# Performance work log

Measured on AMD Instinct MI355X. Metric: run time of the kernel, lower is better.

The kernel has to match this reference:

```python
import jax, jax.numpy as jnp
import numpy as np

ETA = 0.15
LAM = 0.05
K = 6


def setup_inputs() -> dict:
    key = jax.random.key(0)
    ks = jax.random.split(key, 9)
    Bsz, L, d, hidden = 32, 8192, 64, 256
    scale = lambda fan_in: 1.0 / np.sqrt(fan_in)
    return {
        "A": jax.random.normal(ks[0], (Bsz, L, d), jnp.float32),
        "B": jax.random.normal(ks[1], (Bsz, L, d), jnp.float32),
        "q": jax.random.normal(ks[2], (Bsz, L, d), jnp.float32),
        "W1": jax.random.normal(ks[3], (2 * d, hidden), jnp.float32) * scale(2 * d),
        "b1": jax.random.normal(ks[4], (hidden,), jnp.float32) * 0.01,
        "W2": jax.random.normal(ks[5], (hidden, d), jnp.float32) * scale(hidden),
        "b2": jax.random.normal(ks[6], (d,), jnp.float32) * 0.01,
        "Wq": jax.random.normal(ks[7], (d, d), jnp.float32) * scale(d),
        "bq": jax.random.normal(ks[8], (d,), jnp.float32) * 0.01,
    }


def _smooth1d(x):
    return x - LAM * (2.0 * x - jnp.roll(x, 1, axis=1) - jnp.roll(x, -1, axis=1))


def reference(A, B, q, W1, b1, W2, b2, Wq, bq):
    # mu_net: Linear -> ReLU -> Linear -> Softplus on concat([A,B])
    h = jnp.concatenate([A, B], axis=-1)  # [B, L, 2d]
    mu = jax.nn.softplus(jax.nn.relu(h @ W1 + b1) @ W2 + b2)  # [B, L, d]
    gate = jnp.tanh(q @ Wq + bq)
    mu = mu * (1.0 + 0.5 * gate)

    hA, hB = A, B
    for _ in range(K):
        step = ETA * (mu * (hA - hB))
        hA = _smooth1d(hA - step)
        hB = _smooth1d(hB + step)

    energy = 0.5 * jnp.sum(mu * jnp.square(hA - hB), axis=(1, 2))  # [B]
    return hA, hB, energy
```

## Files before the change

kernel.cpp:

```cpp
#include <hip/hip_runtime.h>
#include <hip/hip_bf16.h>
#include <hip/hip_fp16.h>

#define ETA 0.15f
#define LAM 0.05f

typedef unsigned int uint32;
typedef __attribute__((ext_vector_type(8))) short short8;
typedef __attribute__((ext_vector_type(4))) float floatx4;
typedef __attribute__((ext_vector_type(2))) uint32 uint32x2;
typedef __attribute__((ext_vector_type(4))) _Float16 half4;

static const int BSZ = 32, LL = 8192, DD = 64;
static const int RTOT = BSZ * LL;

static const size_t MU_BYTES = (size_t)RTOT * DD * 2;
static const size_t W1T_OFF  = MU_BYTES;
static const size_t W2T_OFF  = W1T_OFF + 256 * 128 * 2;
static const size_t WQT_OFF  = W2T_OFF + 64 * 256 * 2;

__device__ __forceinline__ unsigned short f2bf(float f) {
    uint32 u = __builtin_bit_cast(uint32, f);
    uint32 r = (u + 0x7FFFu + ((u >> 16) & 1u)) >> 16;
    return (unsigned short)r;
}
__device__ __forceinline__ uint32 cvtpk(float lo, float hi) {
    uint32 r;
    asm("v_cvt_pk_bf16_f32 %0, %1, %2" : "=v"(r) : "v"(lo), "v"(hi));
    return r;
}
__device__ __forceinline__ float fast_softplus(float x) {
    return fmaxf(x, 0.f) + __logf(1.f + __expf(-fabsf(x)));
}
__device__ __forceinline__ float fast_tanh(float x) {
    float t = __expf(-2.f * fabsf(x));
    float r = (1.f - t) / (1.f + t);
    return copysignf(r, x);
}

__global__ void prep_kernel(const float* __restrict__ W1, const float* __restrict__ W2,
                            const float* __restrict__ Wq,
                            unsigned short* __restrict__ w1t, unsigned short* __restrict__ w2t,
                            unsigned short* __restrict__ wqt, float* __restrict__ energy) {
    int tid = blockIdx.x * blockDim.x + threadIdx.x;
    int nth = gridDim.x * blockDim.x;
    for (int i = tid; i < 256 * 128; i += nth) { int n = i >> 7, k = i & 127; w1t[i] = f2bf(W1[k * 256 + n]); }
    for (int i = tid; i < 64 * 256; i += nth) { int n = i >> 8, k = i & 255; w2t[i] = f2bf(W2[k * 64 + n]); }
    for (int i = tid; i < 64 * 64;  i += nth) { int n = i >> 6, k = i & 63;  wqt[i] = f2bf(Wq[k * 64 + n]); }
    if (tid < 32) energy[tid] = 0.f;
}

__global__ __launch_bounds__(256) void mlp_kernel(
    const float* __restrict__ A, const float* __restrict__ B, const float* __restrict__ Q,
    const float* __restrict__ b1, const float* __restrict__ b2, const float* __restrict__ bq,
    const unsigned short* __restrict__ w1t, const unsigned short* __restrict__ w2t,
    const unsigned short* __restrict__ wqt, _Float16* __restrict__ mu_out) {
    __shared__ char lds[32768];
    unsigned short* Xs = (unsigned short*)(lds);
    unsigned short* Qs = (unsigned short*)(lds + 17408);
    unsigned short* Zs = (unsigned short*)(lds);

    const int tid = threadIdx.x;
    const int lane = tid & 63;
    const int w = tid >> 6;
    const int q4 = lane >> 4;
    const int l16 = lane & 15;
    const int rowbase = blockIdx.x * 64;

    short8 wqf[2];
#pragma unroll
    for (int kt = 0; kt < 2; kt++)
        wqf[kt] = *(const short8*)&wqt[(w * 16 + l16) * 64 + kt * 32 + q4 * 8];
    float b1v4[4];
#pragma unroll
    for (int nt = 0; nt < 4; nt++) b1v4[nt] = b1[(w * 4 + nt) * 16 + l16];
    const int ocol = w * 16 + l16;
    const float b2v = b2[ocol], bqv = bq[ocol];

    uint32* Xu = (uint32*)Xs;
    for (int i = tid; i < 64 * 32; i += 256) {
        int r = i >> 5, c = i & 31;
        const float* src = (c < 16) ? (A + (size_t)(rowbase + r) * 64 + c * 4)
                                    : (B + (size_t)(rowbase + r) * 64 + (c - 16) * 4);
        floatx4 v = *(const floatx4*)src;
        uint32x2 u; u.x = cvtpk(v.x, v.y); u.y = cvtpk(v.z, v.w);
        *(uint32x2*)&Xu[r * 68 + c * 2] = u;
    }
    uint32* Qu = (uint32*)Qs;
    for (int i = tid; i < 64 * 16; i += 256) {
        int r = i >> 4, c = i & 15;
        floatx4 v = *(const floatx4*)(Q + (size_t)(rowbase + r) * 64 + c * 4);
        uint32x2 u; u.x = cvtpk(v.x, v.y); u.y = cvtpk(v.z, v.w);
        *(uint32x2*)&Qu[r * 36 + c * 2] = u;
    }
    __syncthreads();

    floatx4 acc3[4];
#pragma unroll
    for (int m = 0; m < 4; m++) acc3[m] = (floatx4){0.f, 0.f, 0.f, 0.f};
    __builtin_amdgcn_s_setprio(1);
#pragma unroll
    for (int m = 0; m < 4; m++)
#pragma unroll
        for (int kt = 0; kt < 2; kt++) {
            short8 aq = *(const short8*)&Qs[(m * 16 + l16) * 72 + kt * 32 + q4 * 8];
            acc3[m] = __builtin_amdgcn_mfma_f32_16x16x32_bf16(aq, wqf[kt], acc3[m], 0, 0, 0);
        }
    __builtin_amdgcn_s_setprio(0);
    short8 ax[4][4];
#pragma unroll
    for (int m = 0; m < 4; m++)
#pragma unroll
        for (int kt = 0; kt < 4; kt++)
            ax[m][kt] = *(const short8*)&Xs[(m * 16 + l16) * 136 + kt * 32 + q4 * 8];
    __syncthreads();

#pragma unroll
    for (int nt = 0; nt < 4; nt++) {
        const int ng = w * 4 + nt;
        short8 wf[4];
#pragma unroll
        for (int kt = 0; kt < 4; kt++)
            wf[kt] = *(const short8*)&w1t[(ng * 16 + l16) * 128 + kt * 32 + q4 * 8];
        floatx4 acc[4];
#pragma unroll
        for (int m = 0; m < 4; m++) acc[m] = (floatx4){0.f, 0.f, 0.f, 0.f};
        __builtin_amdgcn_s_setprio(1);
#pragma unroll
        for (int kt = 0; kt < 4; kt++)
#pragma unroll
            for (int m = 0; m < 4; m++)
                acc[m] = __builtin_amdgcn_mfma_f32_16x16x32_bf16(ax[m][kt], wf[kt], acc[m], 0, 0, 0);
        __builtin_amdgcn_s_setprio(0);
        const int col = ng * 16 + l16;
        const int c8 = col >> 3, c7 = col & 7;
        const float b1v = b1v4[nt];
#pragma unroll
        for (int m = 0; m < 4; m++) {
            float z0 = fmaxf(acc[m][0] + b1v, 0.f);
            float z1 = fmaxf(acc[m][1] + b1v, 0.f);
            float z2 = fmaxf(acc[m][2] + b1v, 0.f);
            float z3 = fmaxf(acc[m][3] + b1v, 0.f);
            uint32 u01 = cvtpk(z0, z1), u23 = cvtpk(z2, z3);
            const int row0 = m * 16 + q4 * 4;
            const int a0 = row0 * 256 + ((c8 ^ (q4 * 2)) << 3) + c7;
            const int a2 = (row0 + 2) * 256 + ((c8 ^ (q4 * 2 + 1)) << 3) + c7;
            Zs[a0]       = (unsigned short)u01;
            Zs[a0 + 256] = (unsigned short)(u01 >> 16);
            Zs[a2]       = (unsigned short)u23;
            Zs[a2 + 256] = (unsigned short)(u23 >> 16);
        }
    }
    short8 w2f[8];
#pragma unroll
    for (int kt = 0; kt < 8; kt++)
        w2f[kt] = *(const short8*)&w2t[(w * 16 + l16) * 256 + kt * 32 + q4 * 8];
    __syncthreads();

    floatx4 acc2[4];
#pragma unroll
    for (int m = 0; m < 4; m++) acc2[m] = (floatx4){0.f, 0.f, 0.f, 0.f};
    const int sxr = (l16 >> 1) & 7;
    __builtin_amdgcn_s_setprio(1);
#pragma unroll
    for (int m = 0; m < 4; m++)
#pragma unroll
        for (int kt = 0; kt < 8; kt++) {
            short8 az = *(const short8*)&Zs[(m * 16 + l16) * 256 + (((kt * 4 + q4) ^ sxr) << 3)];
            acc2[m] = __builtin_amdgcn_mfma_f32_16x16x32_bf16(az, w2f[kt], acc2[m], 0, 0, 0);
        }
    __builtin_amdgcn_s_setprio(0);
#pragma unroll
    for (int m = 0; m < 4; m++)
#pragma unroll
        for (int r = 0; r < 4; r++) {
            int row = m * 16 + q4 * 4 + r;
            float sp = fast_softplus(acc2[m][r] + b2v);
            float g = fast_tanh(acc3[m][r] + bqv);
            float mu = sp * (1.f + 0.5f * g);
            mu_out[(size_t)(rowbase + row) * 64 + ocol] = (_Float16)mu;
        }
}

__global__ __launch_bounds__(256) void iter_kernel(
    const float* __restrict__ A, const float* __restrict__ B, const _Float16* __restrict__ mu_ws,
    float* __restrict__ outA, float* __restrict__ outB, float* __restrict__ energy) {
    __shared__ float ex[2][4][16][64];
    __shared__ float esm[4];
    const int tid = threadIdx.x;
    const int c4 = tid & 15;
    const int g = tid >> 4;
    const int b = blockIdx.y;
    const int s0 = blockIdx.x * 64;
    const size_t bbase = (size_t)b * 8192;
    const int r0 = g * 5;

    floatx4 sv[5], dv[5], fv[5];
#pragma unroll
    for (int i = 0; i < 5; i++) {
        int gl = (s0 + r0 + i + 8192 - 8) & 8191;
        size_t base = (bbase + gl) * 64 + c4 * 4;
        floatx4 av = *(const floatx4*)(A + base);
        floatx4 bv = *(const floatx4*)(B + base);
        half4 m4 = *(const half4*)(mu_ws + base);
        floatx4 mu = __builtin_convertvector(m4, floatx4);
        sv[i] = av + bv;
        dv[i] = av - bv;
        fv[i] = 1.f - (2.f * ETA) * mu;
    }
    for (int it = 0; it < 6; it++) {
#pragma unroll
        for (int i = 0; i < 5; i++) dv[i] *= fv[i];
        const int p = it & 1;
        *(floatx4*)&ex[p][0][g][c4 * 4] = sv[0];
        *(floatx4*)&ex[p][1][g][c4 * 4] = sv[4];
        *(floatx4*)&ex[p][2][g][c4 * 4] = dv[0];
        *(floatx4*)&ex[p][3][g][c4 * 4] = dv[4];
        __syncthreads();
        floatx4 sUp = (g > 0)  ? *(const floatx4*)&ex[p][1][g - 1][c4 * 4] : sv[0];
        floatx4 sDn = (g < 15) ? *(const floatx4*)&ex[p][0][g + 1][c4 * 4] : sv[4];
        floatx4 dUp = (g > 0)  ? *(const floatx4*)&ex[p][3][g - 1][c4 * 4] : dv[0];
        floatx4 dDn = (g < 15) ? *(const floatx4*)&ex[p][2][g + 1][c4 * 4] : dv[4];
        floatx4 prev = sUp, cur = sv[0];
#pragma unroll
        for (int i = 0; i < 5; i++) {
            floatx4 nxt = (i < 4) ? sv[i + 1] : sDn;
            sv[i] = cur - LAM * (2.f * cur - prev - nxt);
            prev = cur; cur = nxt;
        }
        prev = dUp; cur = dv[0];
#pragma unroll
        for (int i = 0; i < 5; i++) {
            floatx4 nxt = (i < 4) ? dv[i + 1] : dDn;
            dv[i] = cur - LAM * (2.f * cur - prev - nxt);
            prev = cur; cur = nxt;
        }
    }
    float e = 0.f;
#pragma unroll
    for (int i = 0; i < 5; i++) {
        int wr = r0 + i;
        if (wr >= 8 && wr < 72) {
            floatx4 d = dv[i];
            floatx4 q = (1.f - fv[i]) * d * d;
            e += q.x + q.y + q.z + q.w;
            size_t gidx = (bbase + s0 + (wr - 8)) * 64 + c4 * 4;
            *(floatx4*)(outA + gidx) = (sv[i] + d) * 0.5f;
            *(floatx4*)(outB + gidx) = (sv[i] - d) * 0.5f;
        }
    }
    e *= 0.25f / ETA;
#pragma unroll
    for (int off = 32; off > 0; off >>= 1) e += __shfl_down(e, off, 64);
    if ((tid & 63) == 0) esm[tid >> 6] = e;
    __syncthreads();
    if (tid == 0) atomicAdd(energy + b, esm[0] + esm[1] + esm[2] + esm[3]);
}

extern "C" void kernel_launch(void* const* d_in, const int* in_sizes, int n_in,
                              void* d_out, int out_size, void* d_ws, size_t ws_size,
                              hipStream_t stream) {
    const float* A  = (const float*)d_in[0];
    const float* B  = (const float*)d_in[1];
    const float* Q  = (const float*)d_in[2];
    const float* W1 = (const float*)d_in[3];
    const float* b1 = (const float*)d_in[4];
    const float* W2 = (const float*)d_in[5];
    const float* b2 = (const float*)d_in[6];
    const float* Wq = (const float*)d_in[7];
    const float* bq = (const float*)d_in[8];

    float* outA = (float*)d_out;
    float* outB = outA + (size_t)RTOT * 64;
    float* energy = outB + (size_t)RTOT * 64;

    char* ws = (char*)d_ws;
    _Float16* mu_ws = (_Float16*)ws;
    unsigned short* w1t = (unsigned short*)(ws + W1T_OFF);
    unsigned short* w2t = (unsigned short*)(ws + W2T_OFF);
    unsigned short* wqt = (unsigned short*)(ws + WQT_OFF);

    hipLaunchKernelGGL(prep_kernel, dim3(64), dim3(256), 0, stream,
                       W1, W2, Wq, w1t, w2t, wqt, energy);
    hipLaunchKernelGGL(mlp_kernel, dim3(RTOT / 64), dim3(256), 0, stream,
                       A, B, Q, b1, b2, bq, w1t, w2t, wqt, mu_ws);
    hipLaunchKernelGGL(iter_kernel, dim3(LL / 64, BSZ), dim3(256), 0, stream,
                       A, B, mu_ws, outA, outB, energy);
}
```

Before: 396.1 us.

## Fuse MLP mu computation into stencil iteration kernel, keeping mu in LDS

Merges the MLP kernel and the iteration kernel into one. Each block computes mu for its 80-row haloed tile, with operands swapped so the MFMA output is transposed, and stores it as fp16 in LDS instead of a global workspace. This removes the fp16 mu write and read-back plus the second read of A and B. In exchange it recomputes the MLP on 16 halo rows per 64-row tile (about 25% extra matmul work), and the larger LDS footprint of about 64 KB limits occupancy to two blocks per CU.

```diff
diff --git a/kernel.cpp b/kernel.cpp
--- a/kernel.cpp
+++ b/kernel.cpp
@@ -1,5 +1,4 @@
 #include <hip/hip_runtime.h>
-#include <hip/hip_bf16.h>
 #include <hip/hip_fp16.h>
 
 #define ETA 0.15f
@@ -14,10 +13,9 @@
 static const int BSZ = 32, LL = 8192, DD = 64;
 static const int RTOT = BSZ * LL;
 
-static const size_t MU_BYTES = (size_t)RTOT * DD * 2;
-static const size_t W1T_OFF  = MU_BYTES;
-static const size_t W2T_OFF  = W1T_OFF + 256 * 128 * 2;
-static const size_t WQT_OFF  = W2T_OFF + 64 * 256 * 2;
+static const size_t W1T_OFF = 0;
+static const size_t W2T_OFF = W1T_OFF + 256 * 128 * 2;
+static const size_t WQT_OFF = W2T_OFF + 64 * 256 * 2;
 
 __device__ __forceinline__ unsigned short f2bf(float f) {
     uint32 u = __builtin_bit_cast(uint32, f);
@@ -50,105 +48,105 @@
     if (tid < 32) energy[tid] = 0.f;
 }
 
-__global__ __launch_bounds__(256) void mlp_kernel(
+__global__ __launch_bounds__(256, 2) void fused_kernel(
     const float* __restrict__ A, const float* __restrict__ B, const float* __restrict__ Q,
     const float* __restrict__ b1, const float* __restrict__ b2, const float* __restrict__ bq,
     const unsigned short* __restrict__ w1t, const unsigned short* __restrict__ w2t,
-    const unsigned short* __restrict__ wqt, _Float16* __restrict__ mu_out) {
-    __shared__ char lds[32768];
+    const unsigned short* __restrict__ wqt,
+    float* __restrict__ outA, float* __restrict__ outB, float* __restrict__ energy) {
+    __shared__ char lds[64048];
     unsigned short* Xs = (unsigned short*)(lds);
-    unsigned short* Qs = (unsigned short*)(lds + 17408);
-    unsigned short* Zs = (unsigned short*)(lds);
+    unsigned short* Qs = (unsigned short*)(lds + 21760);
+    unsigned short* Zs = (unsigned short*)(lds + 21760);
+    _Float16* muS = (_Float16*)(lds);
+    float* exb = (float*)(lds + 11264);
+    float* esm = (float*)(lds + 44032);
 
     const int tid = threadIdx.x;
     const int lane = tid & 63;
     const int w = tid >> 6;
     const int q4 = lane >> 4;
     const int l16 = lane & 15;
-    const int rowbase = blockIdx.x * 64;
+    const int g = tid >> 4;
+    const int c4 = tid & 15;
+    const int bb = blockIdx.y;
+    const int s0 = blockIdx.x * 64;
+    const size_t bbase = (size_t)bb * LL;
 
     short8 wqf[2];
 #pragma unroll
     for (int kt = 0; kt < 2; kt++)
         wqf[kt] = *(const short8*)&wqt[(w * 16 + l16) * 64 + kt * 32 + q4 * 8];
-    float b1v4[4];
-#pragma unroll
-    for (int nt = 0; nt < 4; nt++) b1v4[nt] = b1[(w * 4 + nt) * 16 + l16];
-    const int ocol = w * 16 + l16;
-    const float b2v = b2[ocol], bqv = bq[ocol];
-
+    floatx4 b1q[4];
+#pragma unroll
+    for (int ht = 0; ht < 4; ht++) b1q[ht] = *(const floatx4*)&b1[w * 64 + ht * 16 + q4 * 4];
+    const floatx4 b2q = *(const floatx4*)&b2[w * 16 + q4 * 4];
+    const floatx4 bqq = *(const floatx4*)&bq[w * 16 + q4 * 4];
+
+    floatx4 av[5], bv[5];
     uint32* Xu = (uint32*)Xs;
-    for (int i = tid; i < 64 * 32; i += 256) {
-        int r = i >> 5, c = i & 31;
-        const float* src = (c < 16) ? (A + (size_t)(rowbase + r) * 64 + c * 4)
-                                    : (B + (size_t)(rowbase + r) * 64 + (c - 16) * 4);
-        floatx4 v = *(const floatx4*)src;
-        uint32x2 u; u.x = cvtpk(v.x, v.y); u.y = cvtpk(v.z, v.w);
-        *(uint32x2*)&Xu[r * 68 + c * 2] = u;
-    }
     uint32* Qu = (uint32*)Qs;
-    for (int i = tid; i < 64 * 16; i += 256) {
-        int r = i >> 4, c = i & 15;
-        floatx4 v = *(const floatx4*)(Q + (size_t)(rowbase + r) * 64 + c * 4);
-        uint32x2 u; u.x = cvtpk(v.x, v.y); u.y = cvtpk(v.z, v.w);
-        *(uint32x2*)&Qu[r * 36 + c * 2] = u;
-    }
-    __syncthreads();
-
-    floatx4 acc3[4];
-#pragma unroll
-    for (int m = 0; m < 4; m++) acc3[m] = (floatx4){0.f, 0.f, 0.f, 0.f};
+#pragma unroll
+    for (int i = 0; i < 5; i++) {
+        int wr = g * 5 + i;
+        int gl = (s0 + wr + LL - 8) & (LL - 1);
+        size_t base = (bbase + gl) * 64 + c4 * 4;
+        av[i] = *(const floatx4*)(A + base);
+        bv[i] = *(const floatx4*)(B + base);
+        floatx4 qv = *(const floatx4*)(Q + base);
+        uint32x2 ua; ua.x = cvtpk(av[i].x, av[i].y); ua.y = cvtpk(av[i].z, av[i].w);
+        uint32x2 ub; ub.x = cvtpk(bv[i].x, bv[i].y); ub.y = cvtpk(bv[i].z, bv[i].w);
+        uint32x2 uq; uq.x = cvtpk(qv.x, qv.y);       uq.y = cvtpk(qv.z, qv.w);
+        *(uint32x2*)&Xu[wr * 68 + c4 * 2] = ua;
+        *(uint32x2*)&Xu[wr * 68 + 32 + c4 * 2] = ub;
+        *(uint32x2*)&Qu[wr * 36 + c4 * 2] = uq;
+    }
+    __syncthreads();
+
+    floatx4 acc3[5];
+#pragma unroll
+    for (int nt = 0; nt < 5; nt++) acc3[nt] = (floatx4){0.f, 0.f, 0.f, 0.f};
     __builtin_amdgcn_s_setprio(1);
 #pragma unroll
-    for (int m = 0; m < 4; m++)
+    for (int nt = 0; nt < 5; nt++)
 #pragma unroll
         for (int kt = 0; kt < 2; kt++) {
-            short8 aq = *(const short8*)&Qs[(m * 16 + l16) * 72 + kt * 32 + q4 * 8];
-            acc3[m] = __builtin_amdgcn_mfma_f32_16x16x32_bf16(aq, wqf[kt], acc3[m], 0, 0, 0);
+            short8 aq = *(const short8*)&Qs[(nt * 16 + l16) * 72 + kt * 32 + q4 * 8];
+            acc3[nt] = __builtin_amdgcn_mfma_f32_16x16x32_bf16(wqf[kt], aq, acc3[nt], 0, 0, 0);
         }
     __builtin_amdgcn_s_setprio(0);
-    short8 ax[4][4];
-#pragma unroll
-    for (int m = 0; m < 4; m++)
+    short8 ax[5][4];
+#pragma unroll
+    for (int nt = 0; nt < 5; nt++)
 #pragma unroll
         for (int kt = 0; kt < 4; kt++)
-            ax[m][kt] = *(const short8*)&Xs[(m * 16 + l16) * 136 + kt * 32 + q4 * 8];
-    __syncthreads();
-
-#pragma unroll
-    for (int nt = 0; nt < 4; nt++) {
-        const int ng = w * 4 + nt;
+            ax[nt][kt] = *(const short8*)&Xs[(nt * 16 + l16) * 136 + kt * 32 + q4 * 8];
+    __syncthreads();
+
+#pragma unroll
+    for (int ht = 0; ht < 4; ht++) {
         short8 wf[4];
 #pragma unroll
         for (int kt = 0; kt < 4; kt++)
-            wf[kt] = *(const short8*)&w1t[(ng * 16 + l16) * 128 + kt * 32 + q4 * 8];
-        floatx4 acc[4];
-#pragma unroll
-        for (int m = 0; m < 4; m++) acc[m] = (floatx4){0.f, 0.f, 0.f, 0.f};
+            wf[kt] = *(const short8*)&w1t[(w * 64 + ht * 16 + l16) * 128 + kt * 32 + q4 * 8];
+        floatx4 acc[5];
+#pragma unroll
+        for (int nt = 0; nt < 5; nt++) acc[nt] = (floatx4){0.f, 0.f, 0.f, 0.f};
         __builtin_amdgcn_s_setprio(1);
 #pragma unroll
         for (int kt = 0; kt < 4; kt++)
 #pragma unroll
-            for (int m = 0; m < 4; m++)
-                acc[m] = __builtin_amdgcn_mfma_f32_16x16x32_bf16(ax[m][kt], wf[kt], acc[m], 0, 0, 0);
+            for (int nt = 0; nt < 5; nt++)
+                acc[nt] = __builtin_amdgcn_mfma_f32_16x16x32_bf16(wf[kt], ax[nt][kt], acc[nt], 0, 0, 0);
         __builtin_amdgcn_s_setprio(0);
-        const int col = ng * 16 + l16;
-        const int c8 = col >> 3, c7 = col & 7;
-        const float b1v = b1v4[nt];
-#pragma unroll
-        for (int m = 0; m < 4; m++) {
-            float z0 = fmaxf(acc[m][0] + b1v, 0.f);
-            float z1 = fmaxf(acc[m][1] + b1v, 0.f);
-            float z2 = fmaxf(acc[m][2] + b1v, 0.f);
-            float z3 = fmaxf(acc[m][3] + b1v, 0.f);
-            uint32 u01 = cvtpk(z0, z1), u23 = cvtpk(z2, z3);
-            const int row0 = m * 16 + q4 * 4;
-            const int a0 = row0 * 256 + ((c8 ^ (q4 * 2)) << 3) + c7;
-            const int a2 = (row0 + 2) * 256 + ((c8 ^ (q4 * 2 + 1)) << 3) + c7;
-            Zs[a0]       = (unsigned short)u01;
-            Zs[a0 + 256] = (unsigned short)(u01 >> 16);
-            Zs[a2]       = (unsigned short)u23;
-            Zs[a2 + 256] = (unsigned short)(u23 >> 16);
+#pragma unroll
+        for (int nt = 0; nt < 5; nt++) {
+            float z0 = fmaxf(acc[nt][0] + b1q[ht].x, 0.f);
+            float z1 = fmaxf(acc[nt][1] + b1q[ht].y, 0.f);
+            float z2 = fmaxf(acc[nt][2] + b1q[ht].z, 0.f);
+            float z3 = fmaxf(acc[nt][3] + b1q[ht].w, 0.f);
+            uint32x2 uz; uz.x = cvtpk(z0, z1); uz.y = cvtpk(z2, z3);
+            *(uint32x2*)&Zs[(nt * 16 + l16) * 264 + w * 64 + ht * 16 + q4 * 4] = uz;
         }
     }
     short8 w2f[8];
@@ -157,70 +155,53 @@
         w2f[kt] = *(const short8*)&w2t[(w * 16 + l16) * 256 + kt * 32 + q4 * 8];
     __syncthreads();
 
-    floatx4 acc2[4];
-#pragma unroll
-    for (int m = 0; m < 4; m++) acc2[m] = (floatx4){0.f, 0.f, 0.f, 0.f};
-    const int sxr = (l16 >> 1) & 7;
+    floatx4 acc2[5];
+#pragma unroll
+    for (int nt = 0; nt < 5; nt++) acc2[nt] = (floatx4){0.f, 0.f, 0.f, 0.f};
     __builtin_amdgcn_s_setprio(1);
 #pragma unroll
-    for (int m = 0; m < 4; m++)
+    for (int nt = 0; nt < 5; nt++)
 #pragma unroll
         for (int kt = 0; kt < 8; kt++) {
-            short8 az = *(const short8*)&Zs[(m * 16 + l16) * 256 + (((kt * 4 + q4) ^ sxr) << 3)];
-            acc2[m] = __builtin_amdgcn_mfma_f32_16x16x32_bf16(az, w2f[kt], acc2[m], 0, 0, 0);
+            short8 az = *(const short8*)&Zs[(nt * 16 + l16) * 264 + kt * 32 + q4 * 8];
+            acc2[nt] = __builtin_amdgcn_mfma_f32_16x16x32_bf16(w2f[kt], az, acc2[nt], 0, 0, 0);
         }
     __builtin_amdgcn_s_setprio(0);
 #pragma unroll
-    for (int m = 0; m < 4; m++)
+    for (int nt = 0; nt < 5; nt++) {
+        half4 h;
 #pragma unroll
         for (int r = 0; r < 4; r++) {
-            int row = m * 16 + q4 * 4 + r;
-            float sp = fast_softplus(acc2[m][r] + b2v);
-            float g = fast_tanh(acc3[m][r] + bqv);
-            float mu = sp * (1.f + 0.5f * g);
-            mu_out[(size_t)(rowbase + row) * 64 + ocol] = (_Float16)mu;
-        }
-}
-
-__global__ __launch_bounds__(256) void iter_kernel(
-    const float* __restrict__ A, const float* __restrict__ B, const _Float16* __restrict__ mu_ws,
-    float* __restrict__ outA, float* __restrict__ outB, float* __restrict__ energy) {
-    __shared__ float ex[2][4][16][64];
-    __shared__ float esm[4];
-    const int tid = threadIdx.x;
-    const int c4 = tid & 15;
-    const int g = tid >> 4;
-    const int b = blockIdx.y;
-    const int s0 = blockIdx.x * 64;
-    const size_t bbase = (size_t)b * 8192;
-    const int r0 = g * 5;
+            float sp = fast_softplus(acc2[nt][r] + ((const float*)&b2q)[r]);
+            float gt = fast_tanh(acc3[nt][r] + ((const float*)&bqq)[r]);
+            h[r] = (_Float16)(sp * (1.f + 0.5f * gt));
+        }
+        *(half4*)&muS[(nt * 16 + l16) * 68 + w * 16 + q4 * 4] = h;
+    }
+    __syncthreads();
 
     floatx4 sv[5], dv[5], fv[5];
 #pragma unroll
     for (int i = 0; i < 5; i++) {
-        int gl = (s0 + r0 + i + 8192 - 8) & 8191;
-        size_t base = (bbase + gl) * 64 + c4 * 4;
-        floatx4 av = *(const floatx4*)(A + base);
-        floatx4 bv = *(const floatx4*)(B + base);
-        half4 m4 = *(const half4*)(mu_ws + base);
-        floatx4 mu = __builtin_convertvector(m4, floatx4);
-        sv[i] = av + bv;
-        dv[i] = av - bv;
-        fv[i] = 1.f - (2.f * ETA) * mu;
-    }
+        sv[i] = av[i] + bv[i];
+        dv[i] = av[i] - bv[i];
+        half4 m4 = *(const half4*)&muS[(g * 5 + i) * 68 + c4 * 4];
+        fv[i] = 1.f - (2.f * ETA) * __builtin_convertvector(m4, floatx4);
+    }
+#define EX(p, t, gg) (exb + (((p) * 4 + (t)) * 16 + (gg)) * 64 + c4 * 4)
     for (int it = 0; it < 6; it++) {
 #pragma unroll
         for (int i = 0; i < 5; i++) dv[i] *= fv[i];
         const int p = it & 1;
-        *(floatx4*)&ex[p][0][g][c4 * 4] = sv[0];
-        *(floatx4*)&ex[p][1][g][c4 * 4] = sv[4];
-        *(floatx4*)&ex[p][2][g][c4 * 4] = dv[0];
-        *(floatx4*)&ex[p][3][g][c4 * 4] = dv[4];
+        *(floatx4*)EX(p, 0, g) = sv[0];
+        *(floatx4*)EX(p, 1, g) = sv[4];
+        *(floatx4*)EX(p, 2, g) = dv[0];
+        *(floatx4*)EX(p, 3, g) = dv[4];
         __syncthreads();
-        floatx4 sUp = (g > 0)  ? *(const floatx4*)&ex[p][1][g - 1][c4 * 4] : sv[0];
-        floatx4 sDn = (g < 15) ? *(const floatx4*)&ex[p][0][g + 1][c4 * 4] : sv[4];
-        floatx4 dUp = (g > 0)  ? *(const floatx4*)&ex[p][3][g - 1][c4 * 4] : dv[0];
-        floatx4 dDn = (g < 15) ? *(const floatx4*)&ex[p][2][g + 1][c4 * 4] : dv[4];
+        floatx4 sUp = (g > 0)  ? *(const floatx4*)EX(p, 1, g - 1) : sv[0];
+        floatx4 sDn = (g < 15) ? *(const floatx4*)EX(p, 0, g + 1) : sv[4];
+        floatx4 dUp = (g > 0)  ? *(const floatx4*)EX(p, 3, g - 1) : dv[0];
+        floatx4 dDn = (g < 15) ? *(const floatx4*)EX(p, 2, g + 1) : dv[4];
         floatx4 prev = sUp, cur = sv[0];
 #pragma unroll
         for (int i = 0; i < 5; i++) {
@@ -236,14 +217,15 @@
             prev = cur; cur = nxt;
         }
     }
+#undef EX
     float e = 0.f;
 #pragma unroll
     for (int i = 0; i < 5; i++) {
-        int wr = r0 + i;
+        int wr = g * 5 + i;
         if (wr >= 8 && wr < 72) {
             floatx4 d = dv[i];
-            floatx4 q = (1.f - fv[i]) * d * d;
-            e += q.x + q.y + q.z + q.w;
+            floatx4 qv = (1.f - fv[i]) * d * d;
+            e += qv.x + qv.y + qv.z + qv.w;
             size_t gidx = (bbase + s0 + (wr - 8)) * 64 + c4 * 4;
             *(floatx4*)(outA + gidx) = (sv[i] + d) * 0.5f;
             *(floatx4*)(outB + gidx) = (sv[i] - d) * 0.5f;
@@ -254,7 +236,7 @@
     for (int off = 32; off > 0; off >>= 1) e += __shfl_down(e, off, 64);
     if ((tid & 63) == 0) esm[tid >> 6] = e;
     __syncthreads();
-    if (tid == 0) atomicAdd(energy + b, esm[0] + esm[1] + esm[2] + esm[3]);
+    if (tid == 0) atomicAdd(energy + bb, esm[0] + esm[1] + esm[2] + esm[3]);
 }
 
 extern "C" void kernel_launch(void* const* d_in, const int* in_sizes, int n_in,
@@ -275,15 +257,12 @@
     float* energy = outB + (size_t)RTOT * 64;
 
     char* ws = (char*)d_ws;
-    _Float16* mu_ws = (_Float16*)ws;
     unsigned short* w1t = (unsigned short*)(ws + W1T_OFF);
     unsigned short* w2t = (unsigned short*)(ws + W2T_OFF);
     unsigned short* wqt = (unsigned short*)(ws + WQT_OFF);
 
     hipLaunchKernelGGL(prep_kernel, dim3(64), dim3(256), 0, stream,
                        W1, W2, Wq, w1t, w2t, wqt, energy);
-    hipLaunchKernelGGL(mlp_kernel, dim3(RTOT / 64), dim3(256), 0, stream,
-                       A, B, Q, b1, b2, bq, w1t, w2t, wqt, mu_ws);
-    hipLaunchKernelGGL(iter_kernel, dim3(LL / 64, BSZ), dim3(256), 0, stream,
-                       A, B, mu_ws, outA, outB, energy);
-}
+    hipLaunchKernelGGL(fused_kernel, dim3(LL / 64, BSZ), dim3(256), 0, stream,
+                       A, B, Q, b1, b2, bq, w1t, w2t, wqt, outA, outB, energy);
+}
```

New measurement: 346.6 us. 12.5% less time.
